# Performance work log

Measured on AMD Instinct MI355X. Metric: run time of the kernel, lower is better.

Reference implementation:

```python
import jax, jax.numpy as jnp
import numpy as np

PAD_BIG = 1e20  # matches F.pad(value=1e20) on y2


def setup_inputs() -> dict:
    key = jax.random.key(0)
    k1, k2, k3 = jax.random.split(key, 3)
    N, C, H, W = 2, 256, 96, 96
    x = jax.random.normal(k1, (N, C, H, W), dtype=jnp.float32)
    y = jax.random.normal(k2, (N, C, H, W), dtype=jnp.float32)
    labels = jax.random.randint(k3, (N, 1, H, W), 0, 124, dtype=jnp.int32)
    return {"x": x, "y": y, "labels": labels, "max_distance": 4, "num_class": 124}


def _window_stack(p, md, h, w):
    # p: padded [n, c, h+2*md, w+2*md] -> [n, c, h, w, k*k]; offset order
    # (di-major, dj-minor) matches F.unfold column ordering.
    k = 2 * md + 1
    return jnp.stack(
        [p[:, :, di:di + h, dj:dj + w] for di in range(k) for dj in range(k)],
        axis=-1,
    )


def reference(x, y, labels, max_distance, num_class):
    # x: query embedding [N,C,H,W]; y: prev-frame embedding [N,C,H,W]
    # labels: prev-frame labels [N,1,H,W] int
    n, c, h, w = x.shape
    md = max_distance
    k = 2 * md + 1
    kk = k * k

    x2 = jnp.sum(x * x, axis=1)  # [n,h,w]
    y2 = jnp.sum(y * y, axis=1, keepdims=True)  # [n,1,h,w]

    pad_sp = [(0, 0), (0, 0), (md, md), (md, md)]
    py = jnp.pad(y, pad_sp)                                   # zeros
    py2 = jnp.pad(y2, pad_sp, constant_values=PAD_BIG)
    plab = jnp.pad(labels.astype(jnp.float32), pad_sp, constant_values=-1.0)

    y_off = _window_stack(py, md, h, w)          # [n,c,h,w,kk]
    y2_off = _window_stack(py2, md, h, w)[:, 0]  # [n,h,w,kk]
    lab_off = _window_stack(plab, md, h, w)[:, 0]  # [n,h,w,kk]

    corr = jnp.einsum('nchw,nchwp->nhwp', x, y_off)  # [n,h,w,kk]
    d = x2[..., None] + y2_off - 2.0 * corr
    d = (jax.nn.sigmoid(d) - 0.5) * 2.0              # in (-1, 1)

    gt_ids = jnp.arange(num_class, dtype=jnp.float32)
    # mask: [n,h,w,kk,num_class]; padded label -1 never matches -> fill 1.0
    mask = lab_off[..., None] == gt_ids
    dists = jnp.min(jnp.where(mask, d[..., None], 1.0), axis=3)  # [n,h,w,nc]
    return jnp.transpose(dists, (0, 3, 1, 2))  # [n,num_class,h,w]
```

## Files before the change

### kernel.cpp

```cpp
#include <hip/hip_runtime.h>
#include <stdint.h>

#define Nn 2
#define Cc 256
#define Hh 96
#define Ww 96
#define HW (Hh * Ww)
#define MD 4
#define NC 124
#define TH 4
#define TWD 8
#define NQ (TH * TWD)
#define SH (TH + 2 * MD)
#define SWD (TWD + 2 * MD)
#define NS (SH * SWD)
#define BLK 256
#define NBW (Ww / TWD)
#define NBH (Hh / TH)
#define NBLK (Nn * NBH * NBW)
#define YROW 64
#define XOFF (NS * YROW)
#define BUFSZ (XOFF + NQ * YROW)
#define TBL (NQ * NC)

typedef short short8 __attribute__((ext_vector_type(8)));
typedef float f32x4 __attribute__((ext_vector_type(4)));

__device__ __forceinline__ unsigned fmap(float f) {
    unsigned b = __float_as_uint(f);
    return (b & 0x80000000u) ? ~b : (b | 0x80000000u);
}
__device__ __forceinline__ float funmap(unsigned u) {
    unsigned b = (u & 0x80000000u) ? (u & 0x7fffffffu) : ~u;
    return __uint_as_float(b);
}
__device__ __forceinline__ int swz(int row, int slot) {
    return row * YROW + ((slot ^ ((row >> 1) & 3)) << 4);
}

__global__ __launch_bounds__(BLK, 2) void propnet_fused(
    const float* __restrict__ x, const float* __restrict__ y,
    const int* __restrict__ labels, float* __restrict__ out)
{
    __shared__ __align__(16) float F[32 * NS];
    __shared__ __align__(16) unsigned char B[BUFSZ];
    __shared__ float y2s[NS];
    __shared__ float x2s[NQ];
    __shared__ int   labs[NS];
    unsigned* table = (unsigned*)F;

    const int t = threadIdx.x;

    const int orig = blockIdx.x;
    const int lin  = (orig & 7) * (NBLK / 8) + (orig >> 3);
    const int n    = lin / (NBH * NBW);
    const int rem  = lin - n * (NBH * NBW);
    const int h0   = (rem / NBW) * TH;
    const int w0   = (rem % NBW) * TWD;
    const size_t nb = (size_t)n * Cc * HW;

    if (t < NS) {
        const int sr = t >> 4, sc = t & 15;
        const int gh = h0 - MD + sr, gw = w0 - MD + sc;
        const bool ok = (gh >= 0) && (gh < Hh) && (gw >= 0) && (gw < Ww);
        labs[t] = ok ? labels[(size_t)n * HW + gh * Ww + gw] : -1;
        y2s[t]  = 0.f;
    }
    if (t < NQ) x2s[t] = 0.f;

    const int lane = t & 63;
    const int wid  = t >> 6;

    unsigned yoff[6];
#pragma unroll
    for (int k = 0; k < 6; ++k) {
        const int task = (wid * 6 + k) * 64 + lane;
        const int ch = task / 48;
        const int r  = task - ch * 48;
        const int g  = r >> 2;
        const int sg = r & 3;
        const int gh = min(max(h0 - MD + g, 0), Hh - 1);
        const int ws = min(max(w0 - MD + sg * 4, 0), Ww - 4);
        yoff[k] = (unsigned)((ch * HW + gh * Ww + ws) * 4);
    }
    const char* ybp = (const char*)(y + nb);
    auto stageF = [&](int c) {
        const size_t coff = (size_t)(c * 32) * HW * 4;
#pragma unroll
        for (int k = 0; k < 6; ++k)
            __builtin_amdgcn_global_load_lds(
                (const __attribute__((address_space(1))) unsigned int*)
                    (ybp + coff + yoff[k]),
                (__attribute__((address_space(3))) unsigned int*)
                    ((char*)F + (wid * 6 + k) * 1024),
                16, 0, 0);
    };

    int ppix[3], pwb[3]; const float* pcol[3];
#pragma unroll
    for (int i = 0; i < 3; ++i) {
        const int task = t + 256 * i;
        const int pix  = task % NS;
        const int slot = task / NS;
        ppix[i] = pix;
        pwb[i]  = swz(pix, slot);
        pcol[i] = F + slot * 8 * NS + pix;
    }
    float ysq[3] = {0.f, 0.f, 0.f};
    auto packY = [&]() {
#pragma unroll
        for (int i = 0; i < 3; ++i) {
            float v[8];
#pragma unroll
            for (int j = 0; j < 8; ++j) v[j] = pcol[i][j * NS];
            unsigned pk[4];
#pragma unroll
            for (int j = 0; j < 4; ++j) {
                ysq[i] = fmaf(v[2*j],   v[2*j],   ysq[i]);
                ysq[i] = fmaf(v[2*j+1], v[2*j+1], ysq[i]);
                pk[j] = (__float_as_uint(v[2*j]) >> 16) |
                        (__float_as_uint(v[2*j+1]) & 0xffff0000u);
            }
            *(uint4*)(B + pwb[i]) = make_uint4(pk[0], pk[1], pk[2], pk[3]);
        }
    };

    const bool xw = (t < 128);
    const float* xptr = x; int xoffw = 0, xpix = 0;
    if (xw) {
        xpix = t & 31;
        const int grp = t >> 5;
        const int qr = xpix >> 3, qc = xpix & 7;
        xptr = x + nb + (size_t)(grp * 8) * HW + (size_t)(h0 + qr) * Ww + (w0 + qc);
        xoffw = XOFF + swz(xpix, grp);
    }
    float xsq = 0.f;
    float xv[8];
    auto xload = [&](int c) {
        if (!xw) return;
        const float* p = xptr + (size_t)(c * 32) * HW;
#pragma unroll
        for (int j = 0; j < 8; ++j) xv[j] = p[(size_t)j * HW];
    };
    auto xwrite = [&]() {
        if (!xw) return;
        unsigned pk[4];
#pragma unroll
        for (int j = 0; j < 4; ++j) {
            xsq = fmaf(xv[2*j],   xv[2*j],   xsq);
            xsq = fmaf(xv[2*j+1], xv[2*j+1], xsq);
            pk[j] = (__float_as_uint(xv[2*j]) >> 16) |
                    (__float_as_uint(xv[2*j+1]) & 0xffff0000u);
        }
        *(uint4*)(B + xoffw) = make_uint4(pk[0], pk[1], pk[2], pk[3]);
    };

    const int l15 = lane & 15;
    const int lg  = lane >> 4;
    int aoff[2], boff[3];
#pragma unroll
    for (int mf = 0; mf < 2; ++mf) aoff[mf] = XOFF + swz(mf * 16 + l15, lg);
#pragma unroll
    for (int nf = 0; nf < 3; ++nf) boff[nf] = swz(wid * 48 + nf * 16 + l15, lg);

    f32x4 acc[2][3];
#pragma unroll
    for (int mf = 0; mf < 2; ++mf)
#pragma unroll
        for (int nf = 0; nf < 3; ++nf)
            acc[mf][nf] = (f32x4){0.f, 0.f, 0.f, 0.f};

    auto compute = [&]() {
        short8 a[2], b[3];
#pragma unroll
        for (int mf = 0; mf < 2; ++mf) a[mf] = *(const short8*)(B + aoff[mf]);
#pragma unroll
        for (int nf = 0; nf < 3; ++nf) b[nf] = *(const short8*)(B + boff[nf]);
#pragma unroll
        for (int mf = 0; mf < 2; ++mf)
#pragma unroll
            for (int nf = 0; nf < 3; ++nf)
                acc[mf][nf] = __builtin_amdgcn_mfma_f32_16x16x32_bf16(
                    a[mf], b[nf], acc[mf][nf], 0, 0, 0);
    };

    stageF(0); xload(0);
    __syncthreads();
    packY(); xwrite();
    __syncthreads();
    for (int c = 0; c < 8; ++c) {
        if (c < 7) { stageF(c + 1); xload(c + 1); }
        compute();
        __syncthreads();
        if (c < 7) { packY(); xwrite(); }
        __syncthreads();
    }

#pragma unroll
    for (int i = 0; i < 3; ++i) atomicAdd(&y2s[ppix[i]], ysq[i]);
    if (xw) atomicAdd(&x2s[xpix], xsq);
    for (int i = t; i < TBL; i += BLK) table[i] = 0xBF800000u;
    __syncthreads();

#pragma unroll
    for (int mf = 0; mf < 2; ++mf) {
#pragma unroll
        for (int nf = 0; nf < 3; ++nf) {
#pragma unroll
            for (int r = 0; r < 4; ++r) {
                const int q = mf * 16 + lg * 4 + r;
                const int s = wid * 48 + nf * 16 + l15;
                const int qr = q >> 3, qc = q & 7;
                const int sr = s >> 4, sc = s & 15;
                const int di = sr - qr, dj = sc - qc;
                const int lab = labs[s];
                if (di >= 0 && di <= 2 * MD && dj >= 0 && dj <= 2 * MD &&
                    lab >= 0 && lab < NC) {
                    const float d  = x2s[q] + y2s[s] - 2.0f * acc[mf][nf][r];
                    const float sg = 1.0f / (1.0f + __expf(-d));
                    atomicMin(&table[q * NC + lab], fmap(fmaf(2.0f, sg, -1.0f)));
                }
            }
        }
    }
    __syncthreads();

    const size_t ob = (size_t)n * NC * HW;
    for (int i = t; i < TBL; i += BLK) {
        const int g = i >> 5;
        const int q = i & 31;
        const int qr = q >> 3, qc = q & 7;
        out[ob + (size_t)g * HW + (size_t)(h0 + qr) * Ww + (w0 + qc)] =
            funmap(table[q * NC + g]);
    }
}

extern "C" void kernel_launch(void* const* d_in, const int* in_sizes, int n_in,
                              void* d_out, int out_size, void* d_ws, size_t ws_size,
                              hipStream_t stream) {
    const float* x      = (const float*)d_in[0];
    const float* y      = (const float*)d_in[1];
    const int*   labels = (const int*)d_in[2];
    float*       out    = (float*)d_out;
    (void)in_sizes; (void)n_in; (void)out_size; (void)d_ws; (void)ws_size;

    propnet_fused<<<dim3(NBLK), dim3(BLK), 0, stream>>>(x, y, labels, out);
}
```

Before: 32.34 us.

## Double block threads and stage x through async global-to-LDS loads

Raises the block to 512 threads (8 waves) and splits the MFMA tile so each wave owns one 16-row query fragment and three 16-col neighbor fragments. The x tile now goes through the same async global_load_lds staging as y, and both are packed to bf16 by a unified pack pass instead of separate register loads. This is meant to spread per-block work across more waves and hide the x global-load latency, at the cost of larger blocks, more LDS per block and a higher launch-bounds occupancy target.

```diff
diff --git a/kernel.cpp b/kernel.cpp
--- a/kernel.cpp
+++ b/kernel.cpp
@@ -14,7 +14,7 @@
 #define SH (TH + 2 * MD)
 #define SWD (TWD + 2 * MD)
 #define NS (SH * SWD)
-#define BLK 256
+#define BLK 512
 #define NBW (Ww / TWD)
 #define NBH (Hh / TH)
 #define NBLK (Nn * NBH * NBW)
@@ -22,6 +22,9 @@
 #define XOFF (NS * YROW)
 #define BUFSZ (XOFF + NQ * YROW)
 #define TBL (NQ * NC)
+#define FW (32 * NS)
+#define XFW (32 * NQ)
+#define NPK (NS * 4 + NQ * 4)
 
 typedef short short8 __attribute__((ext_vector_type(8)));
 typedef float f32x4 __attribute__((ext_vector_type(4)));
@@ -38,16 +41,16 @@
     return row * YROW + ((slot ^ ((row >> 1) & 3)) << 4);
 }
 
-__global__ __launch_bounds__(BLK, 2) void propnet_fused(
+__global__ __launch_bounds__(BLK, 6) void propnet_fused(
     const float* __restrict__ x, const float* __restrict__ y,
     const int* __restrict__ labels, float* __restrict__ out)
 {
-    __shared__ __align__(16) float F[32 * NS];
+    __shared__ __align__(16) float FX[FW + XFW];
     __shared__ __align__(16) unsigned char B[BUFSZ];
     __shared__ float y2s[NS];
     __shared__ float x2s[NQ];
     __shared__ int   labs[NS];
-    unsigned* table = (unsigned*)F;
+    unsigned* table = (unsigned*)FX;
 
     const int t = threadIdx.x;
 
@@ -71,10 +74,10 @@
     const int lane = t & 63;
     const int wid  = t >> 6;
 
-    unsigned yoff[6];
-#pragma unroll
-    for (int k = 0; k < 6; ++k) {
-        const int task = (wid * 6 + k) * 64 + lane;
+    unsigned yoff[3];
+#pragma unroll
+    for (int k = 0; k < 3; ++k) {
+        const int task = (wid * 3 + k) * 64 + lane;
         const int ch = task / 48;
         const int r  = task - ch * 48;
         const int g  = r >> 2;
@@ -83,41 +86,70 @@
         const int ws = min(max(w0 - MD + sg * 4, 0), Ww - 4);
         yoff[k] = (unsigned)((ch * HW + gh * Ww + ws) * 4);
     }
+    unsigned xoff = 0;
+    if (wid < 4) {
+        const int task = wid * 64 + lane;
+        const int ch  = task >> 3;
+        const int seg = task & 7;
+        xoff = (unsigned)((ch * HW + (h0 + (seg >> 1)) * Ww + w0 + (seg & 1) * 4) * 4);
+    }
     const char* ybp = (const char*)(y + nb);
-    auto stageF = [&](int c) {
+    const char* xbp = (const char*)(x + nb);
+    auto stage = [&](int c) {
         const size_t coff = (size_t)(c * 32) * HW * 4;
 #pragma unroll
-        for (int k = 0; k < 6; ++k)
+        for (int k = 0; k < 3; ++k)
             __builtin_amdgcn_global_load_lds(
                 (const __attribute__((address_space(1))) unsigned int*)
                     (ybp + coff + yoff[k]),
                 (__attribute__((address_space(3))) unsigned int*)
-                    ((char*)F + (wid * 6 + k) * 1024),
+                    ((char*)FX + (wid * 3 + k) * 1024),
+                16, 0, 0);
+        if (wid < 4)
+            __builtin_amdgcn_global_load_lds(
+                (const __attribute__((address_space(1))) unsigned int*)
+                    (xbp + coff + xoff),
+                (__attribute__((address_space(3))) unsigned int*)
+                    ((char*)FX + FW * 4 + wid * 1024),
                 16, 0, 0);
     };
 
-    int ppix[3], pwb[3]; const float* pcol[3];
-#pragma unroll
-    for (int i = 0; i < 3; ++i) {
-        const int task = t + 256 * i;
-        const int pix  = task % NS;
-        const int slot = task / NS;
-        ppix[i] = pix;
-        pwb[i]  = swz(pix, slot);
-        pcol[i] = F + slot * 8 * NS + pix;
-    }
-    float ysq[3] = {0.f, 0.f, 0.f};
-    auto packY = [&]() {
-#pragma unroll
-        for (int i = 0; i < 3; ++i) {
+    bool pvalid[2], pisy[2]; int ppix[2], pwb[2], pstr[2]; const float* pcol[2];
+#pragma unroll
+    for (int i = 0; i < 2; ++i) {
+        const int task = t + BLK * i;
+        pvalid[i] = task < NPK;
+        pisy[i]   = task < NS * 4;
+        if (pisy[i]) {
+            const int pix  = task % NS;
+            const int slot = task / NS;
+            ppix[i] = pix;
+            pwb[i]  = swz(pix, slot);
+            pcol[i] = FX + slot * 8 * NS + pix;
+            pstr[i] = NS;
+        } else {
+            const int u    = (task - NS * 4) & 127;
+            const int px   = u & 31;
+            const int slot = u >> 5;
+            ppix[i] = px;
+            pwb[i]  = XOFF + swz(px, slot);
+            pcol[i] = FX + FW + slot * 8 * NQ + px;
+            pstr[i] = NQ;
+        }
+    }
+    float psq[2] = {0.f, 0.f};
+    auto pack = [&]() {
+#pragma unroll
+        for (int i = 0; i < 2; ++i) {
+            if (!pvalid[i]) continue;
             float v[8];
 #pragma unroll
-            for (int j = 0; j < 8; ++j) v[j] = pcol[i][j * NS];
+            for (int j = 0; j < 8; ++j) v[j] = pcol[i][j * pstr[i]];
             unsigned pk[4];
 #pragma unroll
             for (int j = 0; j < 4; ++j) {
-                ysq[i] = fmaf(v[2*j],   v[2*j],   ysq[i]);
-                ysq[i] = fmaf(v[2*j+1], v[2*j+1], ysq[i]);
+                psq[i] = fmaf(v[2*j],   v[2*j],   psq[i]);
+                psq[i] = fmaf(v[2*j+1], v[2*j+1], psq[i]);
                 pk[j] = (__float_as_uint(v[2*j]) >> 16) |
                         (__float_as_uint(v[2*j+1]) & 0xffff0000u);
             }
@@ -125,101 +157,61 @@
         }
     };
 
-    const bool xw = (t < 128);
-    const float* xptr = x; int xoffw = 0, xpix = 0;
-    if (xw) {
-        xpix = t & 31;
-        const int grp = t >> 5;
-        const int qr = xpix >> 3, qc = xpix & 7;
-        xptr = x + nb + (size_t)(grp * 8) * HW + (size_t)(h0 + qr) * Ww + (w0 + qc);
-        xoffw = XOFF + swz(xpix, grp);
-    }
-    float xsq = 0.f;
-    float xv[8];
-    auto xload = [&](int c) {
-        if (!xw) return;
-        const float* p = xptr + (size_t)(c * 32) * HW;
-#pragma unroll
-        for (int j = 0; j < 8; ++j) xv[j] = p[(size_t)j * HW];
-    };
-    auto xwrite = [&]() {
-        if (!xw) return;
-        unsigned pk[4];
-#pragma unroll
-        for (int j = 0; j < 4; ++j) {
-            xsq = fmaf(xv[2*j],   xv[2*j],   xsq);
-            xsq = fmaf(xv[2*j+1], xv[2*j+1], xsq);
-            pk[j] = (__float_as_uint(xv[2*j]) >> 16) |
-                    (__float_as_uint(xv[2*j+1]) & 0xffff0000u);
-        }
-        *(uint4*)(B + xoffw) = make_uint4(pk[0], pk[1], pk[2], pk[3]);
-    };
-
     const int l15 = lane & 15;
     const int lg  = lane >> 4;
-    int aoff[2], boff[3];
-#pragma unroll
-    for (int mf = 0; mf < 2; ++mf) aoff[mf] = XOFF + swz(mf * 16 + l15, lg);
-#pragma unroll
-    for (int nf = 0; nf < 3; ++nf) boff[nf] = swz(wid * 48 + nf * 16 + l15, lg);
-
-    f32x4 acc[2][3];
-#pragma unroll
-    for (int mf = 0; mf < 2; ++mf)
+    const int aoff = XOFF + swz((wid >> 2) * 16 + l15, lg);
+    int boff[3];
+#pragma unroll
+    for (int nf = 0; nf < 3; ++nf)
+        boff[nf] = swz((wid & 3) * 48 + nf * 16 + l15, lg);
+
+    f32x4 acc[3];
+#pragma unroll
+    for (int nf = 0; nf < 3; ++nf) acc[nf] = (f32x4){0.f, 0.f, 0.f, 0.f};
+
+    auto compute = [&]() {
+        short8 a = *(const short8*)(B + aoff);
+        short8 b[3];
+#pragma unroll
+        for (int nf = 0; nf < 3; ++nf) b[nf] = *(const short8*)(B + boff[nf]);
 #pragma unroll
         for (int nf = 0; nf < 3; ++nf)
-            acc[mf][nf] = (f32x4){0.f, 0.f, 0.f, 0.f};
-
-    auto compute = [&]() {
-        short8 a[2], b[3];
-#pragma unroll
-        for (int mf = 0; mf < 2; ++mf) a[mf] = *(const short8*)(B + aoff[mf]);
-#pragma unroll
-        for (int nf = 0; nf < 3; ++nf) b[nf] = *(const short8*)(B + boff[nf]);
-#pragma unroll
-        for (int mf = 0; mf < 2; ++mf)
-#pragma unroll
-            for (int nf = 0; nf < 3; ++nf)
-                acc[mf][nf] = __builtin_amdgcn_mfma_f32_16x16x32_bf16(
-                    a[mf], b[nf], acc[mf][nf], 0, 0, 0);
+            acc[nf] = __builtin_amdgcn_mfma_f32_16x16x32_bf16(a, b[nf], acc[nf], 0, 0, 0);
     };
 
-    stageF(0); xload(0);
-    __syncthreads();
-    packY(); xwrite();
+    stage(0);
+    __syncthreads();
+    pack();
     __syncthreads();
     for (int c = 0; c < 8; ++c) {
-        if (c < 7) { stageF(c + 1); xload(c + 1); }
+        if (c < 7) stage(c + 1);
         compute();
         __syncthreads();
-        if (c < 7) { packY(); xwrite(); }
+        if (c < 7) pack();
         __syncthreads();
     }
 
 #pragma unroll
-    for (int i = 0; i < 3; ++i) atomicAdd(&y2s[ppix[i]], ysq[i]);
-    if (xw) atomicAdd(&x2s[xpix], xsq);
+    for (int i = 0; i < 2; ++i)
+        if (pvalid[i]) atomicAdd(pisy[i] ? &y2s[ppix[i]] : &x2s[ppix[i]], psq[i]);
     for (int i = t; i < TBL; i += BLK) table[i] = 0xBF800000u;
     __syncthreads();
 
 #pragma unroll
-    for (int mf = 0; mf < 2; ++mf) {
-#pragma unroll
-        for (int nf = 0; nf < 3; ++nf) {
-#pragma unroll
-            for (int r = 0; r < 4; ++r) {
-                const int q = mf * 16 + lg * 4 + r;
-                const int s = wid * 48 + nf * 16 + l15;
-                const int qr = q >> 3, qc = q & 7;
-                const int sr = s >> 4, sc = s & 15;
-                const int di = sr - qr, dj = sc - qc;
-                const int lab = labs[s];
-                if (di >= 0 && di <= 2 * MD && dj >= 0 && dj <= 2 * MD &&
-                    lab >= 0 && lab < NC) {
-                    const float d  = x2s[q] + y2s[s] - 2.0f * acc[mf][nf][r];
-                    const float sg = 1.0f / (1.0f + __expf(-d));
-                    atomicMin(&table[q * NC + lab], fmap(fmaf(2.0f, sg, -1.0f)));
-                }
+    for (int nf = 0; nf < 3; ++nf) {
+#pragma unroll
+        for (int r = 0; r < 4; ++r) {
+            const int q = (wid >> 2) * 16 + lg * 4 + r;
+            const int s = (wid & 3) * 48 + nf * 16 + l15;
+            const int qr = q >> 3, qc = q & 7;
+            const int sr = s >> 4, sc = s & 15;
+            const int di = sr - qr, dj = sc - qc;
+            const int lab = labs[s];
+            if (di >= 0 && di <= 2 * MD && dj >= 0 && dj <= 2 * MD &&
+                lab >= 0 && lab < NC) {
+                const float d  = x2s[q] + y2s[s] - 2.0f * acc[nf][r];
+                const float sg = 1.0f / (1.0f + __expf(-d));
+                atomicMin(&table[q * NC + lab], fmap(fmaf(2.0f, sg, -1.0f)));
             }
         }
     }
```

New measurement: 31.13 us. 1.04x faster.

## Double-buffer async LDS staging of x and y with two-deep prefetch

Applied to the files above, without the earlier changes.

The query embedding x now goes straight into LDS through global_load_lds, like y, instead of going through registers. The fp32 staging buffer is doubled so channel chunks c+1 and c+2 are in flight while chunk c is packed to bf16 and fed to MFMA. The two __syncthreads per iteration become explicit vmcnt/lgkmcnt waits around raw s_barriers, which aims to hide global-load latency behind compute. In exchange, LDS use per block roughly doubles, which could limit occupancy, and the hand-written waitcnt values depend on every thread issuing exactly seven loads per stage.

```diff
diff --git a/kernel.cpp b/kernel.cpp
--- a/kernel.cpp
+++ b/kernel.cpp
@@ -22,6 +22,9 @@
 #define XOFF (NS * YROW)
 #define BUFSZ (XOFF + NQ * YROW)
 #define TBL (NQ * NC)
+#define FW (32 * NS)
+#define XFW (32 * NQ)
+#define FBUF (FW + XFW)
 
 typedef short short8 __attribute__((ext_vector_type(8)));
 typedef float f32x4 __attribute__((ext_vector_type(4)));
@@ -42,12 +45,12 @@
     const float* __restrict__ x, const float* __restrict__ y,
     const int* __restrict__ labels, float* __restrict__ out)
 {
-    __shared__ __align__(16) float F[32 * NS];
+    __shared__ __align__(16) float F2[2][FBUF];
     __shared__ __align__(16) unsigned char B[BUFSZ];
     __shared__ float y2s[NS];
     __shared__ float x2s[NQ];
     __shared__ int   labs[NS];
-    unsigned* table = (unsigned*)F;
+    unsigned* table = (unsigned*)&F2[0][0];
 
     const int t = threadIdx.x;
 
@@ -71,32 +74,41 @@
     const int lane = t & 63;
     const int wid  = t >> 6;
 
-    unsigned yoff[6];
-#pragma unroll
-    for (int k = 0; k < 6; ++k) {
-        const int task = (wid * 6 + k) * 64 + lane;
-        const int ch = task / 48;
-        const int r  = task - ch * 48;
-        const int g  = r >> 2;
-        const int sg = r & 3;
-        const int gh = min(max(h0 - MD + g, 0), Hh - 1);
-        const int ws = min(max(w0 - MD + sg * 4, 0), Ww - 4);
-        yoff[k] = (unsigned)((ch * HW + gh * Ww + ws) * 4);
-    }
-    const char* ybp = (const char*)(y + nb);
-    auto stageF = [&](int c) {
+    const char* sp[7]; int ld[7];
+#pragma unroll
+    for (int k = 0; k < 7; ++k) {
+        const int m = wid * 7 + k;
+        if (m < 24) {
+            const int task = m * 64 + lane;
+            const int ch = task / 48;
+            const int r  = task - ch * 48;
+            const int g  = r >> 2;
+            const int sg = r & 3;
+            const int gh = min(max(h0 - MD + g, 0), Hh - 1);
+            const int ws = min(max(w0 - MD + sg * 4, 0), Ww - 4);
+            sp[k] = (const char*)(y + nb) + (size_t)(ch * HW + gh * Ww + ws) * 4;
+            ld[k] = m * 1024;
+        } else {
+            const int u  = (m - 24) * 64 + lane;
+            const int ch = u >> 3;
+            const int seg = u & 7;
+            sp[k] = (const char*)(x + nb) +
+                    (size_t)(ch * HW + (h0 + (seg >> 1)) * Ww + w0 + (seg & 1) * 4) * 4;
+            ld[k] = FW * 4 + (m - 24) * 1024;
+        }
+    }
+    auto stage = [&](int b, int c) {
         const size_t coff = (size_t)(c * 32) * HW * 4;
-#pragma unroll
-        for (int k = 0; k < 6; ++k)
+        char* Fb = (char*)F2[b];
+#pragma unroll
+        for (int k = 0; k < 7; ++k)
             __builtin_amdgcn_global_load_lds(
-                (const __attribute__((address_space(1))) unsigned int*)
-                    (ybp + coff + yoff[k]),
-                (__attribute__((address_space(3))) unsigned int*)
-                    ((char*)F + (wid * 6 + k) * 1024),
+                (const __attribute__((address_space(1))) unsigned int*)(sp[k] + coff),
+                (__attribute__((address_space(3))) unsigned int*)(Fb + ld[k]),
                 16, 0, 0);
     };
 
-    int ppix[3], pwb[3]; const float* pcol[3];
+    int pco[3], pwb[3], ppix[3];
 #pragma unroll
     for (int i = 0; i < 3; ++i) {
         const int task = t + 256 * i;
@@ -104,15 +116,25 @@
         const int slot = task / NS;
         ppix[i] = pix;
         pwb[i]  = swz(pix, slot);
-        pcol[i] = F + slot * 8 * NS + pix;
+        pco[i]  = slot * 8 * NS + pix;
+    }
+    const bool xw = (t < 128);
+    int xco = 0, xwb = 0, xpix = 0;
+    if (xw) {
+        xpix = t & 31;
+        const int slot = t >> 5;
+        xco = FW + slot * 8 * NQ + xpix;
+        xwb = XOFF + swz(xpix, slot);
     }
     float ysq[3] = {0.f, 0.f, 0.f};
-    auto packY = [&]() {
+    float xsq = 0.f;
+    auto pack = [&](int b) {
+        const float* Fb = F2[b];
 #pragma unroll
         for (int i = 0; i < 3; ++i) {
             float v[8];
 #pragma unroll
-            for (int j = 0; j < 8; ++j) v[j] = pcol[i][j * NS];
+            for (int j = 0; j < 8; ++j) v[j] = Fb[pco[i] + j * NS];
             unsigned pk[4];
 #pragma unroll
             for (int j = 0; j < 4; ++j) {
@@ -123,36 +145,20 @@
             }
             *(uint4*)(B + pwb[i]) = make_uint4(pk[0], pk[1], pk[2], pk[3]);
         }
-    };
-
-    const bool xw = (t < 128);
-    const float* xptr = x; int xoffw = 0, xpix = 0;
-    if (xw) {
-        xpix = t & 31;
-        const int grp = t >> 5;
-        const int qr = xpix >> 3, qc = xpix & 7;
-        xptr = x + nb + (size_t)(grp * 8) * HW + (size_t)(h0 + qr) * Ww + (w0 + qc);
-        xoffw = XOFF + swz(xpix, grp);
-    }
-    float xsq = 0.f;
-    float xv[8];
-    auto xload = [&](int c) {
-        if (!xw) return;
-        const float* p = xptr + (size_t)(c * 32) * HW;
-#pragma unroll
-        for (int j = 0; j < 8; ++j) xv[j] = p[(size_t)j * HW];
-    };
-    auto xwrite = [&]() {
-        if (!xw) return;
-        unsigned pk[4];
-#pragma unroll
-        for (int j = 0; j < 4; ++j) {
-            xsq = fmaf(xv[2*j],   xv[2*j],   xsq);
-            xsq = fmaf(xv[2*j+1], xv[2*j+1], xsq);
-            pk[j] = (__float_as_uint(xv[2*j]) >> 16) |
-                    (__float_as_uint(xv[2*j+1]) & 0xffff0000u);
-        }
-        *(uint4*)(B + xoffw) = make_uint4(pk[0], pk[1], pk[2], pk[3]);
+        if (xw) {
+            float v[8];
+#pragma unroll
+            for (int j = 0; j < 8; ++j) v[j] = Fb[xco + j * NQ];
+            unsigned pk[4];
+#pragma unroll
+            for (int j = 0; j < 4; ++j) {
+                xsq = fmaf(v[2*j],   v[2*j],   xsq);
+                xsq = fmaf(v[2*j+1], v[2*j+1], xsq);
+                pk[j] = (__float_as_uint(v[2*j]) >> 16) |
+                        (__float_as_uint(v[2*j+1]) & 0xffff0000u);
+            }
+            *(uint4*)(B + xwb) = make_uint4(pk[0], pk[1], pk[2], pk[3]);
+        }
     };
 
     const int l15 = lane & 15;
@@ -184,16 +190,25 @@
                     a[mf], b[nf], acc[mf][nf], 0, 0, 0);
     };
 
-    stageF(0); xload(0);
     __syncthreads();
-    packY(); xwrite();
-    __syncthreads();
+    stage(0, 0);
+    stage(1, 1);
+#pragma unroll
     for (int c = 0; c < 8; ++c) {
-        if (c < 7) { stageF(c + 1); xload(c + 1); }
+        if (c < 7) asm volatile("s_waitcnt vmcnt(7)" ::: "memory");
+        else       asm volatile("s_waitcnt vmcnt(0)" ::: "memory");
+        __builtin_amdgcn_sched_barrier(0);
+        __builtin_amdgcn_s_barrier();
+        __builtin_amdgcn_sched_barrier(0);
+        asm volatile("" ::: "memory");
+        pack(c & 1);
+        asm volatile("s_waitcnt lgkmcnt(0)" ::: "memory");
+        __builtin_amdgcn_sched_barrier(0);
+        __builtin_amdgcn_s_barrier();
+        __builtin_amdgcn_sched_barrier(0);
+        asm volatile("" ::: "memory");
+        if (c < 6) stage(c & 1, c + 2);
         compute();
-        __syncthreads();
-        if (c < 7) { packY(); xwrite(); }
-        __syncthreads();
     }
 
 #pragma unroll
```

Result: slower. 41.30 us (+27.7%).

## Double tile height and stage x via direct global-to-LDS loads

Applied to the files above, without the earlier changes.

Doubles the query tile to 8x8 pixels with 512-thread blocks, so each block's 16x16 y halo covers more queries, which lowers the halo re-read overhead. Each of the 8 waves now computes a 32x64 MFMA sub-tile. The x tile is also loaded asynchronously into LDS with global_load_lds instead of register loads, then packed to bf16 alongside y. The cost is half as many blocks, higher LDS use per block, and more wasted MFMA work outside the diagonal window band.

```diff
diff --git a/kernel.cpp b/kernel.cpp
--- a/kernel.cpp
+++ b/kernel.cpp
@@ -8,19 +8,21 @@
 #define HW (Hh * Ww)
 #define MD 4
 #define NC 124
-#define TH 4
+#define TH 8
 #define TWD 8
 #define NQ (TH * TWD)
 #define SH (TH + 2 * MD)
 #define SWD (TWD + 2 * MD)
 #define NS (SH * SWD)
-#define BLK 256
+#define BLK 512
 #define NBW (Ww / TWD)
 #define NBH (Hh / TH)
 #define NBLK (Nn * NBH * NBW)
 #define YROW 64
-#define XOFF (NS * YROW)
-#define BUFSZ (XOFF + NQ * YROW)
+#define XB (NS * YROW)
+#define BUFSZ (XB + NQ * YROW)
+#define FYW (32 * NS)
+#define FXW (32 * NQ)
 #define TBL (NQ * NC)
 
 typedef short short8 __attribute__((ext_vector_type(8)));
@@ -38,11 +40,11 @@
     return row * YROW + ((slot ^ ((row >> 1) & 3)) << 4);
 }
 
-__global__ __launch_bounds__(BLK, 2) void propnet_fused(
+__global__ __launch_bounds__(BLK, 4) void propnet_fused(
     const float* __restrict__ x, const float* __restrict__ y,
     const int* __restrict__ labels, float* __restrict__ out)
 {
-    __shared__ __align__(16) float F[32 * NS];
+    __shared__ __align__(16) float F[FYW + FXW];
     __shared__ __align__(16) unsigned char B[BUFSZ];
     __shared__ float y2s[NS];
     __shared__ float x2s[NQ];
@@ -71,48 +73,69 @@
     const int lane = t & 63;
     const int wid  = t >> 6;
 
-    unsigned yoff[6];
-#pragma unroll
-    for (int k = 0; k < 6; ++k) {
-        const int task = (wid * 6 + k) * 64 + lane;
-        const int ch = task / 48;
-        const int r  = task - ch * 48;
-        const int g  = r >> 2;
-        const int sg = r & 3;
+    int yghw;
+    {
+        const int g  = lane >> 2;
+        const int sg = lane & 3;
         const int gh = min(max(h0 - MD + g, 0), Hh - 1);
         const int ws = min(max(w0 - MD + sg * 4, 0), Ww - 4);
-        yoff[k] = (unsigned)((ch * HW + gh * Ww + ws) * 4);
-    }
-    const char* ybp = (const char*)(y + nb);
-    auto stageF = [&](int c) {
-        const size_t coff = (size_t)(c * 32) * HW * 4;
-#pragma unroll
-        for (int k = 0; k < 6; ++k)
+        yghw = gh * Ww + ws;
+    }
+    int xsoff;
+    {
+        const int chl = lane >> 4;
+        const int qg  = lane & 15;
+        const int qr  = qg >> 1, qc0 = (qg & 1) * 4;
+        xsoff = chl * HW + (h0 + qr) * Ww + (w0 + qc0);
+    }
+    const float* ybp = y + nb;
+    const float* xbp = x + nb;
+    auto stage = [&](int c) {
+        const size_t coff = (size_t)(c * 32) * HW;
+#pragma unroll
+        for (int k = 0; k < 4; ++k) {
+            const int ch = wid * 4 + k;
             __builtin_amdgcn_global_load_lds(
                 (const __attribute__((address_space(1))) unsigned int*)
-                    (ybp + coff + yoff[k]),
+                    (ybp + coff + (size_t)ch * HW + yghw),
                 (__attribute__((address_space(3))) unsigned int*)
-                    ((char*)F + (wid * 6 + k) * 1024),
+                    ((char*)F + ch * (NS * 4)),
                 16, 0, 0);
+        }
+        __builtin_amdgcn_global_load_lds(
+            (const __attribute__((address_space(1))) unsigned int*)
+                (xbp + coff + (size_t)(wid * 4) * HW + xsoff),
+            (__attribute__((address_space(3))) unsigned int*)
+                ((char*)F + FYW * 4 + wid * 1024),
+            16, 0, 0);
     };
 
-    int ppix[3], pwb[3]; const float* pcol[3];
-#pragma unroll
-    for (int i = 0; i < 3; ++i) {
-        const int task = t + 256 * i;
-        const int pix  = task % NS;
-        const int slot = task / NS;
-        ppix[i] = pix;
-        pwb[i]  = swz(pix, slot);
-        pcol[i] = F + slot * 8 * NS + pix;
-    }
-    float ysq[3] = {0.f, 0.f, 0.f};
-    auto packY = [&]() {
-#pragma unroll
-        for (int i = 0; i < 3; ++i) {
+    int ypx[2], ywb[2], yco[2];
+#pragma unroll
+    for (int i = 0; i < 2; ++i) {
+        const int task = t + BLK * i;
+        const int px   = task & 255;
+        const int slot = task >> 8;
+        ypx[i] = px;
+        ywb[i] = swz(px, slot);
+        yco[i] = slot * 8 * NS + px;
+    }
+    const bool xw = (t < 256);
+    int xpx = 0, xwb = 0, xco = 0;
+    if (xw) {
+        xpx = t & 63;
+        const int slot = t >> 6;
+        xwb = XB + swz(xpx, slot);
+        xco = FYW + slot * 8 * NQ + xpx;
+    }
+    float ysq[2] = {0.f, 0.f};
+    float xsq = 0.f;
+    auto pack = [&]() {
+#pragma unroll
+        for (int i = 0; i < 2; ++i) {
             float v[8];
 #pragma unroll
-            for (int j = 0; j < 8; ++j) v[j] = pcol[i][j * NS];
+            for (int j = 0; j < 8; ++j) v[j] = F[yco[i] + j * NS];
             unsigned pk[4];
 #pragma unroll
             for (int j = 0; j < 4; ++j) {
@@ -121,95 +144,81 @@
                 pk[j] = (__float_as_uint(v[2*j]) >> 16) |
                         (__float_as_uint(v[2*j+1]) & 0xffff0000u);
             }
-            *(uint4*)(B + pwb[i]) = make_uint4(pk[0], pk[1], pk[2], pk[3]);
-        }
-    };
-
-    const bool xw = (t < 128);
-    const float* xptr = x; int xoffw = 0, xpix = 0;
-    if (xw) {
-        xpix = t & 31;
-        const int grp = t >> 5;
-        const int qr = xpix >> 3, qc = xpix & 7;
-        xptr = x + nb + (size_t)(grp * 8) * HW + (size_t)(h0 + qr) * Ww + (w0 + qc);
-        xoffw = XOFF + swz(xpix, grp);
-    }
-    float xsq = 0.f;
-    float xv[8];
-    auto xload = [&](int c) {
-        if (!xw) return;
-        const float* p = xptr + (size_t)(c * 32) * HW;
-#pragma unroll
-        for (int j = 0; j < 8; ++j) xv[j] = p[(size_t)j * HW];
-    };
-    auto xwrite = [&]() {
-        if (!xw) return;
-        unsigned pk[4];
-#pragma unroll
-        for (int j = 0; j < 4; ++j) {
-            xsq = fmaf(xv[2*j],   xv[2*j],   xsq);
-            xsq = fmaf(xv[2*j+1], xv[2*j+1], xsq);
-            pk[j] = (__float_as_uint(xv[2*j]) >> 16) |
-                    (__float_as_uint(xv[2*j+1]) & 0xffff0000u);
-        }
-        *(uint4*)(B + xoffw) = make_uint4(pk[0], pk[1], pk[2], pk[3]);
+            *(uint4*)(B + ywb[i]) = make_uint4(pk[0], pk[1], pk[2], pk[3]);
+        }
+        if (xw) {
+            float v[8];
+#pragma unroll
+            for (int j = 0; j < 8; ++j) v[j] = F[xco + j * NQ];
+            unsigned pk[4];
+#pragma unroll
+            for (int j = 0; j < 4; ++j) {
+                xsq = fmaf(v[2*j],   v[2*j],   xsq);
+                xsq = fmaf(v[2*j+1], v[2*j+1], xsq);
+                pk[j] = (__float_as_uint(v[2*j]) >> 16) |
+                        (__float_as_uint(v[2*j+1]) & 0xffff0000u);
+            }
+            *(uint4*)(B + xwb) = make_uint4(pk[0], pk[1], pk[2], pk[3]);
+        }
     };
 
     const int l15 = lane & 15;
     const int lg  = lane >> 4;
-    int aoff[2], boff[3];
-#pragma unroll
-    for (int mf = 0; mf < 2; ++mf) aoff[mf] = XOFF + swz(mf * 16 + l15, lg);
-#pragma unroll
-    for (int nf = 0; nf < 3; ++nf) boff[nf] = swz(wid * 48 + nf * 16 + l15, lg);
-
-    f32x4 acc[2][3];
+    int aoff[2], boff[4];
 #pragma unroll
     for (int mf = 0; mf < 2; ++mf)
-#pragma unroll
-        for (int nf = 0; nf < 3; ++nf)
+        aoff[mf] = XB + swz((wid >> 2) * 32 + mf * 16 + l15, lg);
+#pragma unroll
+    for (int nf = 0; nf < 4; ++nf)
+        boff[nf] = swz((wid & 3) * 64 + nf * 16 + l15, lg);
+
+    f32x4 acc[2][4];
+#pragma unroll
+    for (int mf = 0; mf < 2; ++mf)
+#pragma unroll
+        for (int nf = 0; nf < 4; ++nf)
             acc[mf][nf] = (f32x4){0.f, 0.f, 0.f, 0.f};
 
     auto compute = [&]() {
-        short8 a[2], b[3];
+        short8 a[2], b[4];
 #pragma unroll
         for (int mf = 0; mf < 2; ++mf) a[mf] = *(const short8*)(B + aoff[mf]);
 #pragma unroll
-        for (int nf = 0; nf < 3; ++nf) b[nf] = *(const short8*)(B + boff[nf]);
+        for (int nf = 0; nf < 4; ++nf) b[nf] = *(const short8*)(B + boff[nf]);
 #pragma unroll
         for (int mf = 0; mf < 2; ++mf)
 #pragma unroll
-            for (int nf = 0; nf < 3; ++nf)
+            for (int nf = 0; nf < 4; ++nf)
                 acc[mf][nf] = __builtin_amdgcn_mfma_f32_16x16x32_bf16(
                     a[mf], b[nf], acc[mf][nf], 0, 0, 0);
     };
 
-    stageF(0); xload(0);
-    __syncthreads();
-    packY(); xwrite();
+    stage(0);
+    __syncthreads();
+    pack();
     __syncthreads();
     for (int c = 0; c < 8; ++c) {
-        if (c < 7) { stageF(c + 1); xload(c + 1); }
+        if (c < 7) stage(c + 1);
         compute();
         __syncthreads();
-        if (c < 7) { packY(); xwrite(); }
+        if (c < 7) pack();
         __syncthreads();
     }
 
 #pragma unroll
-    for (int i = 0; i < 3; ++i) atomicAdd(&y2s[ppix[i]], ysq[i]);
-    if (xw) atomicAdd(&x2s[xpix], xsq);
+    for (int i = 0; i < 2; ++i) atomicAdd(&y2s[ypx[i]], ysq[i]);
+    if (xw) atomicAdd(&x2s[xpx], xsq);
     for (int i = t; i < TBL; i += BLK) table[i] = 0xBF800000u;
     __syncthreads();
 
 #pragma unroll
     for (int mf = 0; mf < 2; ++mf) {
 #pragma unroll
-        for (int nf = 0; nf < 3; ++nf) {
+        for (int nf = 0; nf < 4; ++nf) {
 #pragma unroll
             for (int r = 0; r < 4; ++r) {
-                const int q = mf * 16 + lg * 4 + r;
-                const int s = wid * 48 + nf * 16 + l15;
+                const int q = (wid >> 2) * 32 + mf * 16 + lg * 4 + r;
+                const int s = (wid & 3) * 64 + nf * 16 + l15;
                 const int qr = q >> 3, qc = q & 7;
                 const int sr = s >> 4, sc = s & 15;
                 const int di = sr - qr, dj = sc - qc;
@@ -227,8 +236,8 @@
 
     const size_t ob = (size_t)n * NC * HW;
     for (int i = t; i < TBL; i += BLK) {
-        const int g = i >> 5;
-        const int q = i & 31;
+        const int g = i >> 6;
+        const int q = i & 63;
         const int qr = q >> 3, qc = q & 7;
         out[ob + (size_t)g * HW + (size_t)(h0 + qr) * Ww + (w0 + qc)] =
             funmap(table[q * NC + g]);
```

After: 32.42 us. About the same (+0.2%).
